# Kernel optimization log

Hardware: AMD Instinct MI355X
Metric: run time of the kernel (lower is better)

## Reference

```python
import jax, jax.numpy as jnp
import numpy as np

N = 16777216
C = 2
BINS = 10
MOMENTUM = 0.75


def setup_inputs() -> dict:
    key = jax.random.key(0)
    k1, k2 = jax.random.split(key)
    outputs = jax.random.normal(k1, (N, C), dtype=jnp.float32)
    targets = jax.random.randint(k2, (N,), 0, C, dtype=jnp.int64)
    acc_sum = jnp.zeros((BINS,), dtype=jnp.float32)
    return {"outputs": outputs, "targets": targets, "acc_sum": acc_sum}


def reference(outputs, targets, acc_sum):
    n, c = outputs.shape
    tgt = targets.astype(jnp.int32)
    logp = jax.nn.log_softmax(outputs, axis=1)            # [N, C]
    p_t = jnp.take_along_axis(jnp.exp(logp), tgt[:, None], axis=1)[:, 0]
    # |softmax - onehot| summed over classes == 2 * (1 - p_target)
    g = 2.0 * (1.0 - p_t)                                 # [N], in [0, 2]
    # torch loop covers edges linspace(0,1,bins+1): only g in [0, 1) gets a weight
    bin_idx = jnp.clip(jnp.floor(g * BINS).astype(jnp.int32), 0, BINS - 1)
    valid = g < 1.0
    counts = jax.ops.segment_sum(jnp.where(valid, 1.0, 0.0).astype(jnp.float32),
                                 bin_idx, num_segments=BINS)  # [BINS]
    # acc_sum updated only for non-empty bins (EMA with momentum)
    new_acc = jnp.where(counts > 0, MOMENTUM * acc_sum + (1.0 - MOMENTUM) * counts, acc_sum)
    per_sample_acc = new_acc[bin_idx]
    weights = jnp.where(valid & (counts[bin_idx] > 0),
                        jnp.float32(n) / per_sample_acc,
                        jnp.float32(0.0))                 # [N]
    # cross_entropy(reduction='none') = -log_softmax[target]
    loss = -jnp.take_along_axis(logp, tgt[:, None], axis=1)[:, 0]
    return jnp.mean(loss * weights)
```

## Files before the change

kernel.cpp:

```cpp
#include <hip/hip_runtime.h>

#define BINS   10
#define CSHIFT 26
#define QMASK  0x03FFFFFFu
#define QSCALE 2097152.0f
#define QLN2   1453635.25f
#define GRID   4096
#define TPB    256


__global__ void ghm_zero_ws(unsigned* ws) {
    if (threadIdx.x < 32) ws[threadIdx.x] = 0u;
}

__device__ __forceinline__ void proc1(float o0, float o1, int t, unsigned* A) {
    const float Th[BINS] = {
        2.9444390f, 2.1972246f, 1.7346011f, 1.3862944f, 1.0986123f,
        0.8472979f, 0.6190392f, 0.4054651f, 0.2006707f, 0.0f };
    float s = o0 - o1;
    float d = __int_as_float(__float_as_int(s) ^ (t << 31));
    float em = __expf(-d);
    float qf = fmaf(__log2f(1.0f + em), QLN2, 0.5f);
    unsigned val = (unsigned)qf + (1u << CSHIFT);
    #pragma unroll
    for (int b = 0; b < BINS; ++b)
        A[b] += (d > Th[b]) ? val : 0u;
}

__global__ __launch_bounds__(TPB, 4)
void ghm_main(const float* __restrict__ outs,
              const int*   __restrict__ tgt,
              float*       __restrict__ ws_q,
              unsigned*    __restrict__ ws_c,
              int n) {
    const int tid  = threadIdx.x;
    const int lane = tid & 63;
    const int wv   = tid >> 6;

    unsigned A[BINS];
    #pragma unroll
    for (int b = 0; b < BINS; ++b) A[b] = 0u;

    const int nunits  = n >> 1;
    const int wave_id = blockIdx.x * (TPB / 64) + wv;
    const int base    = wave_id * 512;

    const float4* outs4 = (const float4*)outs;
    const int2*   tgt2  = (const int2*)tgt;

    if (base + 512 <= nunits) {
        float4 o[8]; int2 t[8];
        #pragma unroll
        for (int c = 0; c < 8; ++c) {
            int u = base + c * 64 + lane;
            o[c] = outs4[u];
            t[c] = tgt2[u];
        }
        __builtin_amdgcn_sched_barrier(0);
        #pragma unroll
        for (int c = 0; c < 8; ++c) {
            proc1(o[c].x, o[c].y, t[c].x, A);
            proc1(o[c].z, o[c].w, t[c].y, A);
        }
    } else {
        for (int c = 0; c < 8; ++c) {
            int u = base + c * 64 + lane;
            if (u < nunits) {
                float4 o = outs4[u];
                int2   t = tgt2[u];
                proc1(o.x, o.y, t.x, A);
                proc1(o.z, o.w, t.y, A);
            }
        }
    }
    if ((n & 1) && wave_id == 0 && lane == 0)
        proc1(outs[2 * (n - 1)], outs[2 * (n - 1) + 1], tgt[n - 1], A);

    __shared__ unsigned h[BINS][256];
    __shared__ unsigned s_c[BINS][16];
    __shared__ float    s_q[BINS][16];
    #pragma unroll
    for (int b = 0; b < BINS; ++b) h[b][tid] = A[b];
    __syncthreads();

    if (tid < 16 * BINS) {
        int bin  = tid >> 4;
        int part = tid & 15;
        unsigned c = 0, q = 0;
        #pragma unroll
        for (int j = 0; j < 16; ++j) {
            unsigned v = h[bin][j * 16 + part];
            c += v >> CSHIFT;
            q += v & QMASK;
        }
        s_c[bin][part] = c;
        s_q[bin][part] = (float)q;
    }
    __syncthreads();
    if (tid < BINS) {
        unsigned c = 0; float q = 0.0f;
        #pragma unroll
        for (int j = 0; j < 16; ++j) { c += s_c[tid][j]; q += s_q[tid][j]; }
        if (c) {
            atomicAdd(&ws_c[tid], c);
            atomicAdd(&ws_q[tid], q * (1.0f / QSCALE));
        }
    }
}

__global__ void ghm_final(const float*    __restrict__ ws_q,
                          const unsigned* __restrict__ ws_c,
                          const float*    __restrict__ acc_sum,
                          float* __restrict__ out) {
    if (threadIdx.x == 0) {
        float r = 0.0f, pq = 0.0f;
        unsigned pc = 0u;
        #pragma unroll
        for (int b = 0; b < BINS; ++b) {
            float    cq = ws_q[b];
            unsigned cc = ws_c[b];
            unsigned cnt = cc - pc;
            float    qs  = cq - pq;
            pc = cc; pq = cq;
            if (cnt > 0u) {
                float na = 0.75f * acc_sum[b] + 0.25f * (float)cnt;
                r += qs / na;
            }
        }
        *out = r;
    }
}

extern "C" void kernel_launch(void* const* d_in, const int* in_sizes, int n_in,
                              void* d_out, int out_size, void* d_ws, size_t ws_size,
                              hipStream_t stream) {
    const float* outputs = (const float*)d_in[0];
    const int*   targets = (const int*)d_in[1];
    const float* acc_sum = (const float*)d_in[2];
    int n = in_sizes[1];

    float*    ws_q = (float*)d_ws;
    unsigned* ws_c = (unsigned*)((char*)d_ws + 64);

    ghm_zero_ws<<<1, 64, 0, stream>>>((unsigned*)d_ws);
    ghm_main<<<GRID, TPB, 0, stream>>>(outputs, targets, ws_q, ws_c, n);
    ghm_final<<<1, 64, 0, stream>>>(ws_q, ws_c, acc_sum, (float*)d_out);
}
```

Measured before the change: 244.9 us.

## Stream tiles into LDS with double-buffered async loads in persistent grid

Replaces the one-shot per-wave register loads with a persistent grid of blocks. Each block walks over 1024-sample tiles and prefetches the next tile directly into LDS using global_load_lds while it processes the current one. The goal is to overlap memory fetch with the exp/log and binning arithmetic and to raise occupancy (launch bounds 4→6), cutting launch and tail cost. In exchange it adds a __syncthreads per tile and relies on the async LDS loads having completed at the barrier. The LDS use also grows through a union with the epilogue buffers.

Result: no change. 241.3 us (-1.4%).

```diff
diff --git a/kernel.cpp b/kernel.cpp
--- a/kernel.cpp
+++ b/kernel.cpp
@@ -5,12 +5,19 @@
 #define QMASK  0x03FFFFFFu
 #define QSCALE 2097152.0f
 #define QLN2   1453635.25f
-#define GRID   4096
+#define GRID   1536
 #define TPB    256
+#define TILE   1024
 
 
 __global__ void ghm_zero_ws(unsigned* ws) {
     if (threadIdx.x < 32) ws[threadIdx.x] = 0u;
+}
+
+__device__ __forceinline__ void gld_lds16(const void* g, void* l) {
+    __builtin_amdgcn_global_load_lds(
+        (const __attribute__((address_space(1))) void*)g,
+        (__attribute__((address_space(3))) void*)l, 16, 0, 0);
 }
 
 __device__ __forceinline__ void proc1(float o0, float o1, int t, unsigned* A) {
@@ -27,12 +34,24 @@
         A[b] += (d > Th[b]) ? val : 0u;
 }
 
-__global__ __launch_bounds__(TPB, 4)
+__global__ __launch_bounds__(TPB, 6)
 void ghm_main(const float* __restrict__ outs,
               const int*   __restrict__ tgt,
               float*       __restrict__ ws_q,
               unsigned*    __restrict__ ws_c,
               int n) {
+    __shared__ union {
+        struct {
+            unsigned char o[2][TILE * 8];
+            unsigned char t[2][TILE * 4];
+        } st;
+        struct {
+            unsigned h[BINS][256];
+            unsigned c[BINS][16];
+            float    q[BINS][16];
+        } ep;
+    } sh;
+
     const int tid  = threadIdx.x;
     const int lane = tid & 63;
     const int wv   = tid >> 6;
@@ -41,46 +60,54 @@
     #pragma unroll
     for (int b = 0; b < BINS; ++b) A[b] = 0u;
 
-    const int nunits  = n >> 1;
-    const int wave_id = blockIdx.x * (TPB / 64) + wv;
-    const int base    = wave_id * 512;
+    const int ntiles = n >> 10;
 
-    const float4* outs4 = (const float4*)outs;
-    const int2*   tgt2  = (const int2*)tgt;
+    const char* outs_b = (const char*)outs;
+    const char* tgt_b  = (const char*)tgt;
+    #define STAGE(tile, pb)                                                     \
+        do {                                                                    \
+            const char* go = outs_b + ((size_t)(tile) << 13) + (wv << 11)       \
+                             + (lane << 4);                                     \
+            char*       lo = (char*)sh.st.o[pb] + (wv << 11);                   \
+            gld_lds16(go, lo);                                                  \
+            gld_lds16(go + 1024, lo + 1024);                                    \
+            const char* gt = tgt_b + ((size_t)(tile) << 12) + (wv << 10)        \
+                             + (lane << 4);                                     \
+            gld_lds16(gt, (char*)sh.st.t[pb] + (wv << 10));                     \
+        } while (0)
 
-    if (base + 512 <= nunits) {
-        float4 o[8]; int2 t[8];
-        #pragma unroll
-        for (int c = 0; c < 8; ++c) {
-            int u = base + c * 64 + lane;
-            o[c] = outs4[u];
-            t[c] = tgt2[u];
-        }
-        __builtin_amdgcn_sched_barrier(0);
-        #pragma unroll
-        for (int c = 0; c < 8; ++c) {
-            proc1(o[c].x, o[c].y, t[c].x, A);
-            proc1(o[c].z, o[c].w, t[c].y, A);
-        }
-    } else {
-        for (int c = 0; c < 8; ++c) {
-            int u = base + c * 64 + lane;
-            if (u < nunits) {
-                float4 o = outs4[u];
-                int2   t = tgt2[u];
-                proc1(o.x, o.y, t.x, A);
-                proc1(o.z, o.w, t.y, A);
-            }
-        }
+    int t  = blockIdx.x;
+    int pb = 0;
+    if (t < ntiles) STAGE(t, 0);
+    __syncthreads();
+
+    for (; t < ntiles; t += gridDim.x) {
+        int tn = t + gridDim.x;
+        if (tn < ntiles) STAGE(tn, pb ^ 1);
+
+        const float4* o4 = (const float4*)sh.st.o[pb];
+        const int4*   t4 = (const int4*)sh.st.t[pb];
+        float4 a  = o4[2 * tid];
+        float4 bq = o4[2 * tid + 1];
+        int4   tv = t4[tid];
+        proc1(a.x,  a.y,  tv.x, A);
+        proc1(a.z,  a.w,  tv.y, A);
+        proc1(bq.x, bq.y, tv.z, A);
+        proc1(bq.z, bq.w, tv.w, A);
+
+        __syncthreads();
+        pb ^= 1;
     }
-    if ((n & 1) && wave_id == 0 && lane == 0)
-        proc1(outs[2 * (n - 1)], outs[2 * (n - 1) + 1], tgt[n - 1], A);
 
-    __shared__ unsigned h[BINS][256];
-    __shared__ unsigned s_c[BINS][16];
-    __shared__ float    s_q[BINS][16];
+    int rem = ntiles << 10;
+    if (blockIdx.x == 0) {
+        for (int s = rem + tid; s < n; s += TPB)
+            proc1(outs[2 * s], outs[2 * s + 1], tgt[s], A);
+    }
+
+    __syncthreads();
     #pragma unroll
-    for (int b = 0; b < BINS; ++b) h[b][tid] = A[b];
+    for (int b = 0; b < BINS; ++b) sh.ep.h[b][tid] = A[b];
     __syncthreads();
 
     if (tid < 16 * BINS) {
@@ -89,18 +116,18 @@
         unsigned c = 0, q = 0;
         #pragma unroll
         for (int j = 0; j < 16; ++j) {
-            unsigned v = h[bin][j * 16 + part];
+            unsigned v = sh.ep.h[bin][j * 16 + part];
             c += v >> CSHIFT;
             q += v & QMASK;
         }
-        s_c[bin][part] = c;
-        s_q[bin][part] = (float)q;
+        sh.ep.c[bin][part] = c;
+        sh.ep.q[bin][part] = (float)q;
     }
     __syncthreads();
     if (tid < BINS) {
         unsigned c = 0; float q = 0.0f;
         #pragma unroll
-        for (int j = 0; j < 16; ++j) { c += s_c[tid][j]; q += s_q[tid][j]; }
+        for (int j = 0; j < 16; ++j) { c += sh.ep.c[tid][j]; q += sh.ep.q[tid][j]; }
         if (c) {
             atomicAdd(&ws_c[tid], c);
             atomicAdd(&ws_q[tid], q * (1.0f / QSCALE));
```
